# Performance work log

Measured on AMD Instinct MI355X. Metric: run time of the kernel, lower is better.

Reference implementation:

```python
import jax, jax.numpy as jnp
import numpy as np

NUM_HEADS = 8
NUM_LEVELS = 4
NUM_POINTS = 4


def _grid_sample(v, grid):
    """Bilinear grid_sample, padding_mode='zeros', align_corners=False.
    v: (N, C, H, W), grid: (N, Hg, Wg, 2) with grid[...,0]=x, grid[...,1]=y in [-1,1].
    Returns (N, C, Hg, Wg)."""
    N, C, H, W = v.shape
    Hg, Wg = grid.shape[1], grid.shape[2]
    x = ((grid[..., 0] + 1.0) * W - 1.0) * 0.5
    y = ((grid[..., 1] + 1.0) * H - 1.0) * 0.5
    x0 = jnp.floor(x)
    y0 = jnp.floor(y)
    x1 = x0 + 1.0
    y1 = y0 + 1.0
    wx1 = x - x0
    wx0 = 1.0 - wx1
    wy1 = y - y0
    wy0 = 1.0 - wy1
    vf = v.reshape(N, C, H * W)

    def corner(xi, yi, w):
        valid = (xi >= 0) & (xi < W) & (yi >= 0) & (yi < H)
        xi_c = jnp.clip(xi, 0, W - 1).astype(jnp.int32)
        yi_c = jnp.clip(yi, 0, H - 1).astype(jnp.int32)
        idx = (yi_c * W + xi_c).reshape(N, 1, Hg * Wg)
        g = jnp.take_along_axis(vf, idx, axis=2).reshape(N, C, Hg, Wg)
        return g * (w * valid.astype(v.dtype))[:, None]

    return (corner(x0, y0, wx0 * wy0) + corner(x1, y0, wx1 * wy0)
            + corner(x0, y1, wx0 * wy1) + corner(x1, y1, wx1 * wy1))


def setup_inputs() -> dict:
    rng = jax.random.key(0)
    ks = jax.random.split(rng, 6)
    bs, num_q, embed = 1, 40000, 256
    num_kv = NUM_LEVELS * NUM_POINTS  # 16, enforced by the module's asserts
    return {
        "query": jax.random.normal(ks[0], (bs, num_q, embed), jnp.float32),
        "key": jax.random.normal(ks[1], (bs, num_kv, embed), jnp.float32),
        "value": jax.random.normal(ks[2], (bs, num_kv, embed), jnp.float32),
        "reference_points": jax.random.uniform(ks[3], (bs, num_q, NUM_LEVELS, 2), jnp.float32),
        "spatial_shapes": np.array([[1, 2], [2, 2], [2, 3], [1, 2]], dtype=np.int32),  # (h,w), sums to 16
        "W_so": jax.random.normal(ks[4], (embed, NUM_HEADS * NUM_LEVELS * NUM_POINTS * 2), jnp.float32) * 0.02,
        "b_so": jax.random.normal(ks[5], (NUM_HEADS * NUM_LEVELS * NUM_POINTS * 2,), jnp.float32) * 0.02,
    }


def reference(query, key, value, reference_points, spatial_shapes, W_so, b_so):
    b, nq, embed = query.shape
    h, l, p = NUM_HEADS, NUM_LEVELS, NUM_POINTS
    d = embed // h
    ss = np.asarray(spatial_shapes)  # static (l, 2) (h, w)

    # sampling offsets: (b, nq, h, p, l, 2)  -- note (p, l) order per the original view
    off = (query @ W_so + b_so).reshape(b, nq, h, p, l, 2)

    # NOTE: to_Q/to_K/to_V outputs are overwritten in the original (dead code);
    # attention uses the raw query/key reshaped per-head.
    q = query.reshape(b, nq, h, d)
    k = key.reshape(b, -1, h, d)
    v = value.reshape(b, -1, h, d)
    attn = jax.nn.softmax(jnp.einsum('bqhd,bkhd->bqhk', q, k), axis=-1)
    attn = attn.reshape(b, nq, h, l, p)

    # normalize offsets by (w, h) per level, add reference points, then
    # reinterpret (p, l) axes as (l, p) via a plain reshape (faithful to .view)
    norm = jnp.asarray(np.stack([ss[:, 1], ss[:, 0]], axis=-1), dtype=query.dtype)  # (l, 2)
    loc = reference_points[:, :, None, None, :, :] + off / norm  # (b, nq, h, p, l, 2)
    loc = loc.reshape(b, nq, h, l, p, 2)
    grids = 2.0 * loc - 1.0

    sampled = []
    start = 0
    for lev in range(l):
        H_, W_ = int(ss[lev, 0]), int(ss[lev, 1])
        v_l = v[:, start:start + H_ * W_].transpose(0, 2, 3, 1).reshape(b * h, d, H_, W_)
        start += H_ * W_
        g_l = grids[:, :, :, lev].transpose(0, 2, 1, 3, 4).reshape(b * h, nq, p, 2)
        sampled.append(_grid_sample(v_l, g_l))  # (b*h, d, nq, p)
    sampled = jnp.stack(sampled, axis=-2).reshape(b * h, d, nq, l * p)

    aw = attn.transpose(0, 2, 1, 3, 4).reshape(b * h, 1, nq, l * p)
    out = (sampled * aw).sum(-1).reshape(b, h * d, nq)
    return out.transpose(0, 2, 1)
```

## Files before the change

kernel.cpp:

```cpp
#include <hip/hip_runtime.h>
#include <hip/hip_bf16.h>
#include <stdint.h>


typedef __attribute__((ext_vector_type(8))) short short8;
typedef __attribute__((ext_vector_type(4))) float float4_;

#define SB_OFF 5120
#define LDSTR 40
#define SMEM_BYTES 32768

static __device__ __forceinline__ uint16_t f2bf(float f) {
    union { float f; uint32_t u; } a; a.f = f;
    uint32_t r = a.u + 0x7fffu + ((a.u >> 16) & 1u);
    return (uint16_t)(r >> 16);
}
static __device__ __forceinline__ float bf2f(uint16_t b) {
    union { uint32_t u; float f; } a; a.u = ((uint32_t)b) << 16;
    return a.f;
}

template <int H_, int W_, int ST_>
static __device__ __forceinline__ void scatter(float* ws, float a, float x, float y) {
    float x0f = floorf(x), y0f = floorf(y);
    float fx = x - x0f, fy = y - y0f;
    int ix0 = (int)x0f, iy0 = (int)y0f;
    float xc[W_], yc[H_];
#pragma unroll
    for (int cx = 0; cx < W_; ++cx)
        xc[cx] = (ix0 == cx) ? (1.f - fx) : ((ix0 + 1 == cx) ? fx : 0.f);
#pragma unroll
    for (int cy = 0; cy < H_; ++cy)
        yc[cy] = ((iy0 == cy) ? (1.f - fy) : ((iy0 + 1 == cy) ? fy : 0.f)) * a;
#pragma unroll
    for (int cy = 0; cy < H_; ++cy)
#pragma unroll
        for (int cx = 0; cx < W_; ++cx)
            ws[ST_ + cy * W_ + cx] += xc[cx] * yc[cy];
}

__global__ __launch_bounds__(256) void k_transpose(const float* __restrict__ W,
                                                   uint16_t* __restrict__ WTb) {
    int n = blockIdx.x, k = threadIdx.x;
    WTb[n * 256 + k] = f2bf(W[k * 256 + n]);
}

__global__ __launch_bounds__(512, 4) void k_fused(const float* __restrict__ q,
                                                  const float* __restrict__ key,
                                                  const float* __restrict__ value,
                                                  const float* __restrict__ refp,
                                                  const uint16_t* __restrict__ WTb,
                                                  const float* __restrict__ bso,
                                                  float* __restrict__ out) {
    __shared__ __align__(16) char smem[SMEM_BYTES];
    short* sA = (short*)smem;
    short* sB = (short*)(smem + SB_OFF);

    int t = threadIdx.x;
    int w = t >> 6, l = t & 63;
    int qbase = blockIdx.x * 64;
    int qa = qbase + l;
    int g = l >> 4, lrow = l & 15, lk = g * 8;

    int wm = w >> 2, wn = w & 3;
    int ar = t >> 3, ak = t & 7;
    int bn = t >> 1, bh = (t & 1) * 16;
    float4_ acc[2][4];
#pragma unroll
    for (int i = 0; i < 2; ++i)
#pragma unroll
        for (int j = 0; j < 4; ++j) acc[i][j] = (float4_)0.f;

    for (int ks = 0; ks < 8; ++ks) {
        __syncthreads();
        {
            float4_ v = *(const float4_*)(q + (size_t)(qbase + ar) * 256 + ks * 32 + ak * 4);
            uint32_t p0 = (uint32_t)f2bf(v.x) | ((uint32_t)f2bf(v.y) << 16);
            uint32_t p1 = (uint32_t)f2bf(v.z) | ((uint32_t)f2bf(v.w) << 16);
            uint32_t* dst = (uint32_t*)&sA[ar * LDSTR + ak * 4];
            dst[0] = p0; dst[1] = p1;
        }
        {
            const short8* src = (const short8*)(WTb + bn * 256 + ks * 32 + bh);
            *(short8*)&sB[bn * LDSTR + bh]     = src[0];
            *(short8*)&sB[bn * LDSTR + bh + 8] = src[1];
        }
        __syncthreads();
        short8 af[2], bf[4];
#pragma unroll
        for (int mi = 0; mi < 2; ++mi)
            af[mi] = *(const short8*)&sA[(wm * 32 + mi * 16 + lrow) * LDSTR + lk];
#pragma unroll
        for (int ni = 0; ni < 4; ++ni)
            bf[ni] = *(const short8*)&sB[(wn * 64 + ni * 16 + lrow) * LDSTR + lk];
#pragma unroll
        for (int mi = 0; mi < 2; ++mi)
#pragma unroll
            for (int ni = 0; ni < 4; ++ni)
                acc[mi][ni] = __builtin_amdgcn_mfma_f32_16x16x32_bf16(
                    af[mi], bf[ni], acc[mi][ni], 0, 0, 0);
    }
    __syncthreads();

#pragma unroll
    for (int mi = 0; mi < 2; ++mi)
#pragma unroll
        for (int ni = 0; ni < 4; ++ni) {
            int col = wn * 64 + ni * 16 + lrow;
            float b = bso[col];
            int qrow = wm * 32 + mi * 16 + g * 4;
#pragma unroll
            for (int r = 0; r < 4; ++r) {
                int row = qrow + r;
                *(uint16_t*)(smem + row * 512 + ((col * 2) ^ ((row & 7) << 4))) =
                    f2bf(acc[mi][ni][r] + b);
            }
        }

    float sc[16];
    {
        const float4_* qp = (const float4_*)(q + (size_t)qa * 256 + w * 32);
        float4_ qv[8];
#pragma unroll
        for (int j = 0; j < 8; ++j) qv[j] = qp[j];
#pragma unroll
        for (int kk = 0; kk < 16; ++kk) {
            const float4_* kp = (const float4_*)(key + kk * 256 + w * 32);
            float a = 0.f;
#pragma unroll
            for (int j = 0; j < 8; ++j) {
                float4_ kv = kp[j];
                a += qv[j].x * kv.x + qv[j].y * kv.y + qv[j].z * kv.z + qv[j].w * kv.w;
            }
            sc[kk] = a;
        }
        float m = sc[0];
#pragma unroll
        for (int kk = 1; kk < 16; ++kk) m = fmaxf(m, sc[kk]);
        float s = 0.f;
#pragma unroll
        for (int kk = 0; kk < 16; ++kk) { sc[kk] = __expf(sc[kk] - m); s += sc[kk]; }
        float inv = 1.f / s;
#pragma unroll
        for (int kk = 0; kk < 16; ++kk) sc[kk] *= inv;
    }
    __syncthreads();

    union OvU { short8 v; short s[8]; } ov[4];
#pragma unroll
    for (int i = 0; i < 4; ++i)
        ov[i].v = *(const short8*)(smem + l * 512 + ((w * 64 + i * 16) ^ ((l & 7) << 4)));

    union VbU { short8 v; uint16_t u[8]; } vb[2];
#pragma unroll
    for (int nt = 0; nt < 2; ++nt) {
        if (g < 2) {
            int col = w * 32 + nt * 16 + lrow;
#pragma unroll
            for (int j = 0; j < 8; ++j)
                vb[nt].u[j] = f2bf(value[(g * 8 + j) * 256 + col]);
        } else {
#pragma unroll
            for (int j = 0; j < 8; ++j) vb[nt].u[j] = 0;
        }
    }

    float4_ r01 = *(const float4_*)(refp + (size_t)qa * 8);
    float4_ r23 = *(const float4_*)(refp + (size_t)qa * 8 + 4);
    float rx[4] = {r01.x, r01.z, r23.x, r23.z};
    float ry[4] = {r01.y, r01.w, r23.y, r23.w};

    float ws[14];
#pragma unroll
    for (int j = 0; j < 14; ++j) ws[j] = 0.f;

#define SAMPLE_LP(LP, PP, GH, GW, ST, NW, NH)                                 \
    {                                                                         \
        float ox = bf2f((uint16_t)ov[(2 * (LP)) >> 3].s[(2 * (LP)) & 7]);     \
        float oy = bf2f((uint16_t)ov[(2 * (LP) + 1) >> 3].s[(2 * (LP) + 1) & 7]); \
        float x = (rx[PP] + ox * (NW)) * (float)(GW)-0.5f;                    \
        float y = (ry[PP] + oy * (NH)) * (float)(GH)-0.5f;                    \
        scatter<GH, GW, ST>(ws, sc[LP], x, y);                                \
    }
    SAMPLE_LP(0, 0, 1, 2, 0, 0.5f, 1.0f)
    SAMPLE_LP(1, 1, 1, 2, 0, 0.5f, 0.5f)
    SAMPLE_LP(2, 2, 1, 2, 0, (1.f / 3.f), 0.5f)
    SAMPLE_LP(3, 3, 1, 2, 0, 0.5f, 1.0f)
    SAMPLE_LP(4, 0, 2, 2, 2, 0.5f, 1.0f)
    SAMPLE_LP(5, 1, 2, 2, 2, 0.5f, 0.5f)
    SAMPLE_LP(6, 2, 2, 2, 2, (1.f / 3.f), 0.5f)
    SAMPLE_LP(7, 3, 2, 2, 2, 0.5f, 1.0f)
    SAMPLE_LP(8, 0, 2, 3, 6, 0.5f, 1.0f)
    SAMPLE_LP(9, 1, 2, 3, 6, 0.5f, 0.5f)
    SAMPLE_LP(10, 2, 2, 3, 6, (1.f / 3.f), 0.5f)
    SAMPLE_LP(11, 3, 2, 3, 6, 0.5f, 1.0f)
    SAMPLE_LP(12, 0, 1, 2, 12, 0.5f, 1.0f)
    SAMPLE_LP(13, 1, 1, 2, 12, 0.5f, 0.5f)
    SAMPLE_LP(14, 2, 1, 2, 12, (1.f / 3.f), 0.5f)
    SAMPLE_LP(15, 3, 1, 2, 12, 0.5f, 1.0f)
#undef SAMPLE_LP

    __syncthreads();

    {
        union PkU { uint32_t u[8]; short8 v2[2]; } pk;
#pragma unroll
        for (int j = 0; j < 7; ++j)
            pk.u[j] = (uint32_t)f2bf(ws[2 * j]) | ((uint32_t)f2bf(ws[2 * j + 1]) << 16);
        pk.u[7] = 0;
        *(short8*)(smem + t * 48)      = pk.v2[0];
        *(short8*)(smem + t * 48 + 16) = pk.v2[1];
    }
    __syncthreads();

    {
        union ZU { uint32_t u[4]; short8 v; } az;
        az.u[0] = 0; az.u[1] = 0; az.u[2] = 0; az.u[3] = 0;
        float4_ acc2[4][2];
#pragma unroll
        for (int i = 0; i < 4; ++i)
#pragma unroll
            for (int j = 0; j < 2; ++j) acc2[i][j] = (float4_)0.f;
#pragma unroll
        for (int mt = 0; mt < 4; ++mt) {
            short8 af = (g < 2)
                ? *(const short8*)(smem + (w * 64 + mt * 16 + lrow) * 48 + g * 16)
                : az.v;
#pragma unroll
            for (int nt = 0; nt < 2; ++nt)
                acc2[mt][nt] = __builtin_amdgcn_mfma_f32_16x16x32_bf16(
                    af, vb[nt].v, acc2[mt][nt], 0, 0, 0);
        }
#pragma unroll
        for (int mt = 0; mt < 4; ++mt)
#pragma unroll
            for (int nt = 0; nt < 2; ++nt)
#pragma unroll
                for (int r = 0; r < 4; ++r)
                    out[(size_t)(qbase + mt * 16 + g * 4 + r) * 256
                        + w * 32 + nt * 16 + lrow] = acc2[mt][nt][r];
    }
}

extern "C" void kernel_launch(void* const* d_in, const int* in_sizes, int n_in,
                              void* d_out, int out_size, void* d_ws, size_t ws_size,
                              hipStream_t stream) {
    (void)in_sizes; (void)n_in; (void)out_size; (void)ws_size;
    const float* query = (const float*)d_in[0];
    const float* key   = (const float*)d_in[1];
    const float* value = (const float*)d_in[2];
    const float* refp  = (const float*)d_in[3];
    const float* Wso   = (const float*)d_in[5];
    const float* bso   = (const float*)d_in[6];
    uint16_t* WTb = (uint16_t*)d_ws;

    hipLaunchKernelGGL(k_transpose, dim3(256), dim3(256), 0, stream, Wso, WTb);
    hipLaunchKernelGGL(k_fused, dim3(625), dim3(512), 0, stream,
                       query, key, value, refp, WTb, bso, (float*)d_out);
}
```

Before: 70.51 us.

## Halve query tile to 32 per block and register-prefetch next GEMM k-slice

Each block now handles 32 queries with 256 threads instead of 64 queries with 512, doubling the grid to 1250 blocks and cutting LDS use so more blocks fit per CU. The q and W tiles for the next k-step are loaded into registers while the current step computes, hiding global latency behind the MFMA work. Work is remapped so each thread covers a (query, head) pair and each wave does two heads in the value MFMA stage. The cost is that W tiles are reloaded by twice as many blocks, and value is converted twice per wave.

```diff
diff --git a/kernel.cpp b/kernel.cpp
--- a/kernel.cpp
+++ b/kernel.cpp
@@ -6,9 +6,9 @@
 typedef __attribute__((ext_vector_type(8))) short short8;
 typedef __attribute__((ext_vector_type(4))) float float4_;
 
-#define SB_OFF 5120
 #define LDSTR 40
-#define SMEM_BYTES 32768
+#define SB_OFF 2560
+#define SMEM_BYTES 23040
 
 static __device__ __forceinline__ uint16_t f2bf(float f) {
     union { float f; uint32_t u; } a; a.f = f;
@@ -45,7 +45,7 @@
     WTb[n * 256 + k] = f2bf(W[k * 256 + n]);
 }
 
-__global__ __launch_bounds__(512, 4) void k_fused(const float* __restrict__ q,
+__global__ __launch_bounds__(256, 6) void k_fused(const float* __restrict__ q,
                                                   const float* __restrict__ key,
                                                   const float* __restrict__ value,
                                                   const float* __restrict__ refp,
@@ -58,41 +58,49 @@
 
     int t = threadIdx.x;
     int w = t >> 6, l = t & 63;
-    int qbase = blockIdx.x * 64;
-    int qa = qbase + l;
     int g = l >> 4, lrow = l & 15, lk = g * 8;
-
-    int wm = w >> 2, wn = w & 3;
+    int qbase = blockIdx.x * 32;
+    int h2 = t >> 5, ql = t & 31;
+    int qa = qbase + ql;
+
     int ar = t >> 3, ak = t & 7;
-    int bn = t >> 1, bh = (t & 1) * 16;
     float4_ acc[2][4];
 #pragma unroll
     for (int i = 0; i < 2; ++i)
 #pragma unroll
         for (int j = 0; j < 4; ++j) acc[i][j] = (float4_)0.f;
+
+    float4_ pa = *(const float4_*)(q + (size_t)(qbase + ar) * 256 + ak * 4);
+    short8 pb[4];
+#pragma unroll
+    for (int j = 0; j < 4; ++j)
+        pb[j] = *(const short8*)(WTb + t * 256 + j * 8);
 
     for (int ks = 0; ks < 8; ++ks) {
         __syncthreads();
         {
-            float4_ v = *(const float4_*)(q + (size_t)(qbase + ar) * 256 + ks * 32 + ak * 4);
-            uint32_t p0 = (uint32_t)f2bf(v.x) | ((uint32_t)f2bf(v.y) << 16);
-            uint32_t p1 = (uint32_t)f2bf(v.z) | ((uint32_t)f2bf(v.w) << 16);
+            uint32_t p0 = (uint32_t)f2bf(pa.x) | ((uint32_t)f2bf(pa.y) << 16);
+            uint32_t p1 = (uint32_t)f2bf(pa.z) | ((uint32_t)f2bf(pa.w) << 16);
             uint32_t* dst = (uint32_t*)&sA[ar * LDSTR + ak * 4];
             dst[0] = p0; dst[1] = p1;
-        }
-        {
-            const short8* src = (const short8*)(WTb + bn * 256 + ks * 32 + bh);
-            *(short8*)&sB[bn * LDSTR + bh]     = src[0];
-            *(short8*)&sB[bn * LDSTR + bh + 8] = src[1];
+#pragma unroll
+            for (int j = 0; j < 4; ++j)
+                *(short8*)&sB[t * LDSTR + j * 8] = pb[j];
+        }
+        if (ks < 7) {
+            pa = *(const float4_*)(q + (size_t)(qbase + ar) * 256 + (ks + 1) * 32 + ak * 4);
+#pragma unroll
+            for (int j = 0; j < 4; ++j)
+                pb[j] = *(const short8*)(WTb + t * 256 + (ks + 1) * 32 + j * 8);
         }
         __syncthreads();
         short8 af[2], bf[4];
 #pragma unroll
         for (int mi = 0; mi < 2; ++mi)
-            af[mi] = *(const short8*)&sA[(wm * 32 + mi * 16 + lrow) * LDSTR + lk];
+            af[mi] = *(const short8*)&sA[(mi * 16 + lrow) * LDSTR + lk];
 #pragma unroll
         for (int ni = 0; ni < 4; ++ni)
-            bf[ni] = *(const short8*)&sB[(wn * 64 + ni * 16 + lrow) * LDSTR + lk];
+            bf[ni] = *(const short8*)&sB[(w * 64 + ni * 16 + lrow) * LDSTR + lk];
 #pragma unroll
         for (int mi = 0; mi < 2; ++mi)
 #pragma unroll
@@ -106,9 +114,9 @@
     for (int mi = 0; mi < 2; ++mi)
 #pragma unroll
         for (int ni = 0; ni < 4; ++ni) {
-            int col = wn * 64 + ni * 16 + lrow;
+            int col = w * 64 + ni * 16 + lrow;
             float b = bso[col];
-            int qrow = wm * 32 + mi * 16 + g * 4;
+            int qrow = mi * 16 + g * 4;
 #pragma unroll
             for (int r = 0; r < 4; ++r) {
                 int row = qrow + r;
@@ -118,22 +126,27 @@
         }
 
     float sc[16];
-    {
-        const float4_* qp = (const float4_*)(q + (size_t)qa * 256 + w * 32);
-        float4_ qv[8];
-#pragma unroll
-        for (int j = 0; j < 8; ++j) qv[j] = qp[j];
+#pragma unroll
+    for (int kk = 0; kk < 16; ++kk) sc[kk] = 0.f;
+#pragma unroll
+    for (int half = 0; half < 2; ++half) {
+        const float4_* qp = (const float4_*)(q + (size_t)qa * 256 + h2 * 32 + half * 16);
+        float4_ qv[4];
+#pragma unroll
+        for (int j = 0; j < 4; ++j) qv[j] = qp[j];
 #pragma unroll
         for (int kk = 0; kk < 16; ++kk) {
-            const float4_* kp = (const float4_*)(key + kk * 256 + w * 32);
+            const float4_* kp = (const float4_*)(key + kk * 256 + h2 * 32 + half * 16);
             float a = 0.f;
 #pragma unroll
-            for (int j = 0; j < 8; ++j) {
+            for (int j = 0; j < 4; ++j) {
                 float4_ kv = kp[j];
                 a += qv[j].x * kv.x + qv[j].y * kv.y + qv[j].z * kv.z + qv[j].w * kv.w;
             }
-            sc[kk] = a;
-        }
+            sc[kk] += a;
+        }
+    }
+    {
         float m = sc[0];
 #pragma unroll
         for (int kk = 1; kk < 16; ++kk) m = fmaxf(m, sc[kk]);
@@ -149,21 +162,7 @@
     union OvU { short8 v; short s[8]; } ov[4];
 #pragma unroll
     for (int i = 0; i < 4; ++i)
-        ov[i].v = *(const short8*)(smem + l * 512 + ((w * 64 + i * 16) ^ ((l & 7) << 4)));
-
-    union VbU { short8 v; uint16_t u[8]; } vb[2];
-#pragma unroll
-    for (int nt = 0; nt < 2; ++nt) {
-        if (g < 2) {
-            int col = w * 32 + nt * 16 + lrow;
-#pragma unroll
-            for (int j = 0; j < 8; ++j)
-                vb[nt].u[j] = f2bf(value[(g * 8 + j) * 256 + col]);
-        } else {
-#pragma unroll
-            for (int j = 0; j < 8; ++j) vb[nt].u[j] = 0;
-        }
-    }
+        ov[i].v = *(const short8*)(smem + ql * 512 + ((h2 * 64 + i * 16) ^ ((ql & 7) << 4)));
 
     float4_ r01 = *(const float4_*)(refp + (size_t)qa * 8);
     float4_ r23 = *(const float4_*)(refp + (size_t)qa * 8 + 4);
@@ -174,13 +173,13 @@
 #pragma unroll
     for (int j = 0; j < 14; ++j) ws[j] = 0.f;
 
-#define SAMPLE_LP(LP, PP, GH, GW, ST, NW, NH)                                 \
-    {                                                                         \
-        float ox = bf2f((uint16_t)ov[(2 * (LP)) >> 3].s[(2 * (LP)) & 7]);     \
+#define SAMPLE_LP(LP, PP, GH, GW, ST, NW, NH)                                     \
+    {                                                                             \
+        float ox = bf2f((uint16_t)ov[(2 * (LP)) >> 3].s[(2 * (LP)) & 7]);         \
         float oy = bf2f((uint16_t)ov[(2 * (LP) + 1) >> 3].s[(2 * (LP) + 1) & 7]); \
-        float x = (rx[PP] + ox * (NW)) * (float)(GW)-0.5f;                    \
-        float y = (ry[PP] + oy * (NH)) * (float)(GH)-0.5f;                    \
-        scatter<GH, GW, ST>(ws, sc[LP], x, y);                                \
+        float x = (rx[PP] + ox * (NW)) * (float)(GW)-0.5f;                        \
+        float y = (ry[PP] + oy * (NH)) * (float)(GH)-0.5f;                        \
+        scatter<GH, GW, ST>(ws, sc[LP], x, y);                                    \
     }
     SAMPLE_LP(0, 0, 1, 2, 0, 0.5f, 1.0f)
     SAMPLE_LP(1, 1, 1, 2, 0, 0.5f, 0.5f)
@@ -216,29 +215,45 @@
     {
         union ZU { uint32_t u[4]; short8 v; } az;
         az.u[0] = 0; az.u[1] = 0; az.u[2] = 0; az.u[3] = 0;
-        float4_ acc2[4][2];
-#pragma unroll
-        for (int i = 0; i < 4; ++i)
-#pragma unroll
-            for (int j = 0; j < 2; ++j) acc2[i][j] = (float4_)0.f;
-#pragma unroll
-        for (int mt = 0; mt < 4; ++mt) {
-            short8 af = (g < 2)
-                ? *(const short8*)(smem + (w * 64 + mt * 16 + lrow) * 48 + g * 16)
-                : az.v;
-#pragma unroll
-            for (int nt = 0; nt < 2; ++nt)
-                acc2[mt][nt] = __builtin_amdgcn_mfma_f32_16x16x32_bf16(
-                    af, vb[nt].v, acc2[mt][nt], 0, 0, 0);
-        }
-#pragma unroll
-        for (int mt = 0; mt < 4; ++mt)
-#pragma unroll
-            for (int nt = 0; nt < 2; ++nt)
-#pragma unroll
-                for (int r = 0; r < 4; ++r)
-                    out[(size_t)(qbase + mt * 16 + g * 4 + r) * 256
-                        + w * 32 + nt * 16 + lrow] = acc2[mt][nt][r];
+#pragma unroll
+        for (int hh = 0; hh < 2; ++hh) {
+            int h = 2 * w + hh;
+            union VbU { short8 v; uint16_t u[8]; } vb[2];
+#pragma unroll
+            for (int nt = 0; nt < 2; ++nt) {
+                if (g < 2) {
+                    int col = h * 32 + nt * 16 + lrow;
+#pragma unroll
+                    for (int j = 0; j < 8; ++j)
+                        vb[nt].u[j] = f2bf(value[(g * 8 + j) * 256 + col]);
+                } else {
+                    vb[nt].v = az.v;
+                }
+            }
+            float4_ acc2[2][2];
+#pragma unroll
+            for (int i = 0; i < 2; ++i)
+#pragma unroll
+                for (int j = 0; j < 2; ++j) acc2[i][j] = (float4_)0.f;
+#pragma unroll
+            for (int mt = 0; mt < 2; ++mt) {
+                short8 af = (g < 2)
+                    ? *(const short8*)(smem + (h * 32 + mt * 16 + lrow) * 48 + g * 16)
+                    : az.v;
+#pragma unroll
+                for (int nt = 0; nt < 2; ++nt)
+                    acc2[mt][nt] = __builtin_amdgcn_mfma_f32_16x16x32_bf16(
+                        af, vb[nt].v, acc2[mt][nt], 0, 0, 0);
+            }
+#pragma unroll
+            for (int mt = 0; mt < 2; ++mt)
+#pragma unroll
+                for (int nt = 0; nt < 2; ++nt)
+#pragma unroll
+                    for (int r = 0; r < 4; ++r)
+                        out[(size_t)(qbase + mt * 16 + g * 4 + r) * 256
+                            + h * 32 + nt * 16 + lrow] = acc2[mt][nt][r];
+        }
     }
 }
 
@@ -255,6 +270,6 @@
     uint16_t* WTb = (uint16_t*)d_ws;
 
     hipLaunchKernelGGL(k_transpose, dim3(256), dim3(256), 0, stream, Wso, WTb);
-    hipLaunchKernelGGL(k_fused, dim3(625), dim3(512), 0, stream,
+    hipLaunchKernelGGL(k_fused, dim3(1250), dim3(256), 0, stream,
                        query, key, value, refp, WTb, bso, (float*)d_out);
 }
```

After: 167.4 us. +137.4%, slower.

## Restructure into single-wave blocks with pre-swizzled MFMA fragment tables for W and value

Applied to the files above, without the earlier changes.

A prep kernel now converts W_so and value into bf16 tables already in MFMA B-fragment order. The fused kernel runs as one 64-thread wave per 16 queries instead of 512 threads per 64 queries. It reads B fragments straight from global memory with no LDS staging or barriers, and each lane handles two heads for softmax and sampling. This removes block-wide syncs and LDS tiling of the projection, and raises the block count. In exchange, W fragments are re-read from global/L2 by every block and the work per wave grows.

```diff
diff --git a/kernel.cpp b/kernel.cpp
--- a/kernel.cpp
+++ b/kernel.cpp
@@ -6,9 +6,9 @@
 typedef __attribute__((ext_vector_type(8))) short short8;
 typedef __attribute__((ext_vector_type(4))) float float4_;
 
-#define SB_OFF 5120
-#define LDSTR 40
-#define SMEM_BYTES 32768
+#define SOFF_B 0
+#define WSF_B 8192
+#define SMEM_BYTES 14336
 
 static __device__ __forceinline__ uint16_t f2bf(float f) {
     union { float f; uint32_t u; } a; a.f = f;
@@ -39,129 +39,73 @@
             ws[ST_ + cy * W_ + cx] += xc[cx] * yc[cy];
 }
 
-__global__ __launch_bounds__(256) void k_transpose(const float* __restrict__ W,
-                                                   uint16_t* __restrict__ WTb) {
-    int n = blockIdx.x, k = threadIdx.x;
-    WTb[n * 256 + k] = f2bf(W[k * 256 + n]);
-}
-
-__global__ __launch_bounds__(512, 4) void k_fused(const float* __restrict__ q,
-                                                  const float* __restrict__ key,
-                                                  const float* __restrict__ value,
-                                                  const float* __restrict__ refp,
-                                                  const uint16_t* __restrict__ WTb,
-                                                  const float* __restrict__ bso,
-                                                  float* __restrict__ out) {
+__global__ __launch_bounds__(256) void k_prep(const float* __restrict__ W,
+                                              const float* __restrict__ value,
+                                              uint16_t* __restrict__ tab) {
+    int tid = threadIdx.x, b = blockIdx.x;
+    if (b < 32) {
+        int f = b * 256 + tid;
+        int l = f & 63, nt = (f >> 6) & 15, ks = (f >> 10) & 7;
+        int col = nt * 16 + (l & 15);
+        int kb = ks * 32 + (l >> 4) * 8;
+        uint16_t* dst = tab + (size_t)f * 8;
+#pragma unroll
+        for (int j = 0; j < 8; ++j) dst[j] = f2bf(W[(size_t)(kb + j) * 256 + col]);
+    } else {
+        int f = (b - 32) * 256 + tid;
+        int l = f & 63, nt2 = f >> 6;
+        int col = nt2 * 16 + (l & 15);
+        int g = l >> 4;
+        uint16_t* dst = tab + 65536 + (size_t)f * 8;
+#pragma unroll
+        for (int j = 0; j < 8; ++j)
+            dst[j] = (g < 2) ? f2bf(value[(size_t)(g * 8 + j) * 256 + col]) : (uint16_t)0;
+    }
+}
+
+__global__ __launch_bounds__(64) void k_fused(const float* __restrict__ q,
+                                              const float* __restrict__ key,
+                                              const float* __restrict__ refp,
+                                              const uint16_t* __restrict__ Wfrag,
+                                              const uint16_t* __restrict__ vfrag,
+                                              const float* __restrict__ bso,
+                                              float* __restrict__ out) {
     __shared__ __align__(16) char smem[SMEM_BYTES];
-    short* sA = (short*)smem;
-    short* sB = (short*)(smem + SB_OFF);
-
-    int t = threadIdx.x;
-    int w = t >> 6, l = t & 63;
-    int qbase = blockIdx.x * 64;
-    int qa = qbase + l;
-    int g = l >> 4, lrow = l & 15, lk = g * 8;
-
-    int wm = w >> 2, wn = w & 3;
-    int ar = t >> 3, ak = t & 7;
-    int bn = t >> 1, bh = (t & 1) * 16;
-    float4_ acc[2][4];
-#pragma unroll
-    for (int i = 0; i < 2; ++i)
-#pragma unroll
-        for (int j = 0; j < 4; ++j) acc[i][j] = (float4_)0.f;
-
-    for (int ks = 0; ks < 8; ++ks) {
-        __syncthreads();
-        {
-            float4_ v = *(const float4_*)(q + (size_t)(qbase + ar) * 256 + ks * 32 + ak * 4);
-            uint32_t p0 = (uint32_t)f2bf(v.x) | ((uint32_t)f2bf(v.y) << 16);
-            uint32_t p1 = (uint32_t)f2bf(v.z) | ((uint32_t)f2bf(v.w) << 16);
-            uint32_t* dst = (uint32_t*)&sA[ar * LDSTR + ak * 4];
-            dst[0] = p0; dst[1] = p1;
-        }
-        {
-            const short8* src = (const short8*)(WTb + bn * 256 + ks * 32 + bh);
-            *(short8*)&sB[bn * LDSTR + bh]     = src[0];
-            *(short8*)&sB[bn * LDSTR + bh + 8] = src[1];
-        }
-        __syncthreads();
-        short8 af[2], bf[4];
-#pragma unroll
-        for (int mi = 0; mi < 2; ++mi)
-            af[mi] = *(const short8*)&sA[(wm * 32 + mi * 16 + lrow) * LDSTR + lk];
-#pragma unroll
-        for (int ni = 0; ni < 4; ++ni)
-            bf[ni] = *(const short8*)&sB[(wn * 64 + ni * 16 + lrow) * LDSTR + lk];
-#pragma unroll
-        for (int mi = 0; mi < 2; ++mi)
-#pragma unroll
-            for (int ni = 0; ni < 4; ++ni)
-                acc[mi][ni] = __builtin_amdgcn_mfma_f32_16x16x32_bf16(
-                    af[mi], bf[ni], acc[mi][ni], 0, 0, 0);
-    }
-    __syncthreads();
-
-#pragma unroll
-    for (int mi = 0; mi < 2; ++mi)
-#pragma unroll
-        for (int ni = 0; ni < 4; ++ni) {
-            int col = wn * 64 + ni * 16 + lrow;
-            float b = bso[col];
-            int qrow = wm * 32 + mi * 16 + g * 4;
-#pragma unroll
-            for (int r = 0; r < 4; ++r) {
-                int row = qrow + r;
-                *(uint16_t*)(smem + row * 512 + ((col * 2) ^ ((row & 7) << 4))) =
-                    f2bf(acc[mi][ni][r] + b);
+    int l = threadIdx.x;
+    int g = l >> 4, lr = l & 15;
+    int qb = blockIdx.x * 16;
+    int qa = qb + lr;
+
+    for (int np = 0; np < 2; ++np) {
+        float4_ acc[8];
+#pragma unroll
+        for (int i = 0; i < 8; ++i) acc[i] = (float4_)0.f;
+#pragma unroll
+        for (int ks = 0; ks < 8; ++ks) {
+            const float4_* ap = (const float4_*)(q + (size_t)(qb + lr) * 256 + ks * 32 + g * 8);
+            float4_ a0 = ap[0], a1 = ap[1];
+            union { uint32_t u[4]; short8 v; } af;
+            af.u[0] = (uint32_t)f2bf(a0.x) | ((uint32_t)f2bf(a0.y) << 16);
+            af.u[1] = (uint32_t)f2bf(a0.z) | ((uint32_t)f2bf(a0.w) << 16);
+            af.u[2] = (uint32_t)f2bf(a1.x) | ((uint32_t)f2bf(a1.y) << 16);
+            af.u[3] = (uint32_t)f2bf(a1.z) | ((uint32_t)f2bf(a1.w) << 16);
+#pragma unroll
+            for (int nt = 0; nt < 8; ++nt) {
+                short8 bf = *(const short8*)(Wfrag
+                    + ((size_t)(ks * 16 + np * 8 + nt) * 64 + l) * 8);
+                acc[nt] = __builtin_amdgcn_mfma_f32_16x16x32_bf16(af.v, bf, acc[nt], 0, 0, 0);
             }
         }
-
-    float sc[16];
-    {
-        const float4_* qp = (const float4_*)(q + (size_t)qa * 256 + w * 32);
-        float4_ qv[8];
-#pragma unroll
-        for (int j = 0; j < 8; ++j) qv[j] = qp[j];
-#pragma unroll
-        for (int kk = 0; kk < 16; ++kk) {
-            const float4_* kp = (const float4_*)(key + kk * 256 + w * 32);
-            float a = 0.f;
-#pragma unroll
-            for (int j = 0; j < 8; ++j) {
-                float4_ kv = kp[j];
-                a += qv[j].x * kv.x + qv[j].y * kv.y + qv[j].z * kv.z + qv[j].w * kv.w;
+#pragma unroll
+        for (int nt = 0; nt < 8; ++nt) {
+            int col = (np * 8 + nt) * 16 + lr;
+            float b = bso[col];
+#pragma unroll
+            for (int r = 0; r < 4; ++r) {
+                int row = g * 4 + r;
+                *(uint16_t*)(smem + SOFF_B + row * 512 + ((col * 2) ^ ((row & 7) << 4))) =
+                    f2bf(acc[nt][r] + b);
             }
-            sc[kk] = a;
-        }
-        float m = sc[0];
-#pragma unroll
-        for (int kk = 1; kk < 16; ++kk) m = fmaxf(m, sc[kk]);
-        float s = 0.f;
-#pragma unroll
-        for (int kk = 0; kk < 16; ++kk) { sc[kk] = __expf(sc[kk] - m); s += sc[kk]; }
-        float inv = 1.f / s;
-#pragma unroll
-        for (int kk = 0; kk < 16; ++kk) sc[kk] *= inv;
-    }
-    __syncthreads();
-
-    union OvU { short8 v; short s[8]; } ov[4];
-#pragma unroll
-    for (int i = 0; i < 4; ++i)
-        ov[i].v = *(const short8*)(smem + l * 512 + ((w * 64 + i * 16) ^ ((l & 7) << 4)));
-
-    union VbU { short8 v; uint16_t u[8]; } vb[2];
-#pragma unroll
-    for (int nt = 0; nt < 2; ++nt) {
-        if (g < 2) {
-            int col = w * 32 + nt * 16 + lrow;
-#pragma unroll
-            for (int j = 0; j < 8; ++j)
-                vb[nt].u[j] = f2bf(value[(g * 8 + j) * 256 + col]);
-        } else {
-#pragma unroll
-            for (int j = 0; j < 8; ++j) vb[nt].u[j] = 0;
         }
     }
 
@@ -170,75 +114,122 @@
     float rx[4] = {r01.x, r01.z, r23.x, r23.z};
     float ry[4] = {r01.y, r01.w, r23.y, r23.w};
 
-    float ws[14];
-#pragma unroll
-    for (int j = 0; j < 14; ++j) ws[j] = 0.f;
-
-#define SAMPLE_LP(LP, PP, GH, GW, ST, NW, NH)                                 \
+    float wsA[14], wsB[14];
+
+#define SAMPLE_PT(WS, J, PP, GH, GW, ST, NW, NH)                              \
     {                                                                         \
-        float ox = bf2f((uint16_t)ov[(2 * (LP)) >> 3].s[(2 * (LP)) & 7]);     \
-        float oy = bf2f((uint16_t)ov[(2 * (LP) + 1) >> 3].s[(2 * (LP) + 1) & 7]); \
+        float ox = bf2f((uint16_t)ovl.s[2 * (J)]);                            \
+        float oy = bf2f((uint16_t)ovl.s[2 * (J) + 1]);                        \
         float x = (rx[PP] + ox * (NW)) * (float)(GW)-0.5f;                    \
         float y = (ry[PP] + oy * (NH)) * (float)(GH)-0.5f;                    \
-        scatter<GH, GW, ST>(ws, sc[LP], x, y);                                \
-    }
-    SAMPLE_LP(0, 0, 1, 2, 0, 0.5f, 1.0f)
-    SAMPLE_LP(1, 1, 1, 2, 0, 0.5f, 0.5f)
-    SAMPLE_LP(2, 2, 1, 2, 0, (1.f / 3.f), 0.5f)
-    SAMPLE_LP(3, 3, 1, 2, 0, 0.5f, 1.0f)
-    SAMPLE_LP(4, 0, 2, 2, 2, 0.5f, 1.0f)
-    SAMPLE_LP(5, 1, 2, 2, 2, 0.5f, 0.5f)
-    SAMPLE_LP(6, 2, 2, 2, 2, (1.f / 3.f), 0.5f)
-    SAMPLE_LP(7, 3, 2, 2, 2, 0.5f, 1.0f)
-    SAMPLE_LP(8, 0, 2, 3, 6, 0.5f, 1.0f)
-    SAMPLE_LP(9, 1, 2, 3, 6, 0.5f, 0.5f)
-    SAMPLE_LP(10, 2, 2, 3, 6, (1.f / 3.f), 0.5f)
-    SAMPLE_LP(11, 3, 2, 3, 6, 0.5f, 1.0f)
-    SAMPLE_LP(12, 0, 1, 2, 12, 0.5f, 1.0f)
-    SAMPLE_LP(13, 1, 1, 2, 12, 0.5f, 0.5f)
-    SAMPLE_LP(14, 2, 1, 2, 12, (1.f / 3.f), 0.5f)
-    SAMPLE_LP(15, 3, 1, 2, 12, 0.5f, 1.0f)
-#undef SAMPLE_LP
-
-    __syncthreads();
+        scatter<GH, GW, ST>(WS, sc[4 * LEV + (J)], x, y);                     \
+    }
+#define DO_PASS(WS, HH)                                                           \
+    {                                                                             \
+        const int h = (HH);                                                       \
+        float sc[16];                                                             \
+        {                                                                         \
+            const float4_* qp = (const float4_*)(q + (size_t)qa * 256 + h * 32);  \
+            float4_ qv[8];                                                        \
+            _Pragma("unroll") for (int j = 0; j < 8; ++j) qv[j] = qp[j];          \
+            _Pragma("unroll") for (int kk = 0; kk < 16; ++kk) {                   \
+                const float4_* kp = (const float4_*)(key + kk * 256 + h * 32);    \
+                float a = 0.f;                                                    \
+                _Pragma("unroll") for (int j = 0; j < 8; ++j) {                   \
+                    float4_ kv = kp[j];                                           \
+                    a += qv[j].x * kv.x + qv[j].y * kv.y + qv[j].z * kv.z         \
+                       + qv[j].w * kv.w;                                          \
+                }                                                                 \
+                sc[kk] = a;                                                       \
+            }                                                                     \
+            float m = sc[0];                                                      \
+            _Pragma("unroll") for (int kk = 1; kk < 16; ++kk) m = fmaxf(m, sc[kk]); \
+            float s = 0.f;                                                        \
+            _Pragma("unroll") for (int kk = 0; kk < 16; ++kk) {                   \
+                sc[kk] = __expf(sc[kk] - m); s += sc[kk];                         \
+            }                                                                     \
+            float inv = 1.f / s;                                                  \
+            _Pragma("unroll") for (int kk = 0; kk < 16; ++kk) sc[kk] *= inv;      \
+        }                                                                         \
+        _Pragma("unroll") for (int j = 0; j < 14; ++j) WS[j] = 0.f;               \
+        union OvU { short8 v; short s[8]; } ovl;                                  \
+        {                                                                         \
+            enum { LEV = 0 };                                                     \
+            ovl.v = *(const short8*)(smem + SOFF_B + lr * 512                     \
+                        + ((h * 64 + LEV * 16) ^ ((lr & 7) << 4)));               \
+            SAMPLE_PT(WS, 0, 0, 1, 2, 0, 0.5f, 1.0f)                              \
+            SAMPLE_PT(WS, 1, 1, 1, 2, 0, 0.5f, 0.5f)                              \
+            SAMPLE_PT(WS, 2, 2, 1, 2, 0, (1.f / 3.f), 0.5f)                       \
+            SAMPLE_PT(WS, 3, 3, 1, 2, 0, 0.5f, 1.0f)                              \
+        }                                                                         \
+        {                                                                         \
+            enum { LEV = 1 };                                                     \
+            ovl.v = *(const short8*)(smem + SOFF_B + lr * 512                     \
+                        + ((h * 64 + LEV * 16) ^ ((lr & 7) << 4)));               \
+            SAMPLE_PT(WS, 0, 0, 2, 2, 2, 0.5f, 1.0f)                              \
+            SAMPLE_PT(WS, 1, 1, 2, 2, 2, 0.5f, 0.5f)                              \
+            SAMPLE_PT(WS, 2, 2, 2, 2, 2, (1.f / 3.f), 0.5f)                       \
+            SAMPLE_PT(WS, 3, 3, 2, 2, 2, 0.5f, 1.0f)                              \
+        }                                                                         \
+        {                                                                         \
+            enum { LEV = 2 };                                                     \
+            ovl.v = *(const short8*)(smem + SOFF_B + lr * 512                     \
+                        + ((h * 64 + LEV * 16) ^ ((lr & 7) << 4)));               \
+            SAMPLE_PT(WS, 0, 0, 2, 3, 6, 0.5f, 1.0f)                              \
+            SAMPLE_PT(WS, 1, 1, 2, 3, 6, 0.5f, 0.5f)                              \
+            SAMPLE_PT(WS, 2, 2, 2, 3, 6, (1.f / 3.f), 0.5f)                       \
+            SAMPLE_PT(WS, 3, 3, 2, 3, 6, 0.5f, 1.0f)                              \
+        }                                                                         \
+        {                                                                         \
+            enum { LEV = 3 };                                                     \
+            ovl.v = *(const short8*)(smem + SOFF_B + lr * 512                     \
+                        + ((h * 64 + LEV * 16) ^ ((lr & 7) << 4)));               \
+            SAMPLE_PT(WS, 0, 0, 1, 2, 12, 0.5f, 1.0f)                             \
+            SAMPLE_PT(WS, 1, 1, 1, 2, 12, 0.5f, 0.5f)                             \
+            SAMPLE_PT(WS, 2, 2, 1, 2, 12, (1.f / 3.f), 0.5f)                      \
+            SAMPLE_PT(WS, 3, 3, 1, 2, 12, 0.5f, 1.0f)                             \
+        }                                                                         \
+    }
+
+    DO_PASS(wsA, g)
+    DO_PASS(wsB, g + 4)
+#undef DO_PASS
+#undef SAMPLE_PT
 
     {
         union PkU { uint32_t u[8]; short8 v2[2]; } pk;
 #pragma unroll
         for (int j = 0; j < 7; ++j)
-            pk.u[j] = (uint32_t)f2bf(ws[2 * j]) | ((uint32_t)f2bf(ws[2 * j + 1]) << 16);
+            pk.u[j] = (uint32_t)f2bf(wsA[2 * j]) | ((uint32_t)f2bf(wsA[2 * j + 1]) << 16);
         pk.u[7] = 0;
-        *(short8*)(smem + t * 48)      = pk.v2[0];
-        *(short8*)(smem + t * 48 + 16) = pk.v2[1];
-    }
-    __syncthreads();
+        *(short8*)(smem + WSF_B + g * 768 + lr * 48)      = pk.v2[0];
+        *(short8*)(smem + WSF_B + g * 768 + lr * 48 + 16) = pk.v2[1];
+#pragma unroll
+        for (int j = 0; j < 7; ++j)
+            pk.u[j] = (uint32_t)f2bf(wsB[2 * j]) | ((uint32_t)f2bf(wsB[2 * j + 1]) << 16);
+        pk.u[7] = 0;
+        *(short8*)(smem + WSF_B + (g + 4) * 768 + lr * 48)      = pk.v2[0];
+        *(short8*)(smem + WSF_B + (g + 4) * 768 + lr * 48 + 16) = pk.v2[1];
+    }
 
     {
         union ZU { uint32_t u[4]; short8 v; } az;
         az.u[0] = 0; az.u[1] = 0; az.u[2] = 0; az.u[3] = 0;
-        float4_ acc2[4][2];
-#pragma unroll
-        for (int i = 0; i < 4; ++i)
-#pragma unroll
-            for (int j = 0; j < 2; ++j) acc2[i][j] = (float4_)0.f;
-#pragma unroll
-        for (int mt = 0; mt < 4; ++mt) {
-            short8 af = (g < 2)
-                ? *(const short8*)(smem + (w * 64 + mt * 16 + lrow) * 48 + g * 16)
+        float4_ z4 = (float4_)0.f;
+#pragma unroll
+        for (int hp = 0; hp < 8; ++hp) {
+            short8 af2 = (g < 2)
+                ? *(const short8*)(smem + WSF_B + hp * 768 + lr * 48 + g * 16)
                 : az.v;
 #pragma unroll
-            for (int nt = 0; nt < 2; ++nt)
-                acc2[mt][nt] = __builtin_amdgcn_mfma_f32_16x16x32_bf16(
-                    af, vb[nt].v, acc2[mt][nt], 0, 0, 0);
+            for (int nt2 = 0; nt2 < 2; ++nt2) {
+                short8 vb = *(const short8*)(vfrag + ((size_t)(hp * 2 + nt2) * 64 + l) * 8);
+                float4_ o = __builtin_amdgcn_mfma_f32_16x16x32_bf16(af2, vb, z4, 0, 0, 0);
+#pragma unroll
+                for (int r = 0; r < 4; ++r)
+                    out[(size_t)(qb + g * 4 + r) * 256 + hp * 32 + nt2 * 16 + lr] = o[r];
+            }
         }
-#pragma unroll
-        for (int mt = 0; mt < 4; ++mt)
-#pragma unroll
-            for (int nt = 0; nt < 2; ++nt)
-#pragma unroll
-                for (int r = 0; r < 4; ++r)
-                    out[(size_t)(qbase + mt * 16 + g * 4 + r) * 256
-                        + w * 32 + nt * 16 + lrow] = acc2[mt][nt][r];
     }
 }
 
@@ -252,9 +243,9 @@
     const float* refp  = (const float*)d_in[3];
     const float* Wso   = (const float*)d_in[5];
     const float* bso   = (const float*)d_in[6];
-    uint16_t* WTb = (uint16_t*)d_ws;
-
-    hipLaunchKernelGGL(k_transpose, dim3(256), dim3(256), 0, stream, Wso, WTb);
-    hipLaunchKernelGGL(k_fused, dim3(625), dim3(512), 0, stream,
-                       query, key, value, refp, WTb, bso, (float*)d_out);
-}
+    uint16_t* tab = (uint16_t*)d_ws;
+
+    hipLaunchKernelGGL(k_prep, dim3(36), dim3(256), 0, stream, Wso, value, tab);
+    hipLaunchKernelGGL(k_fused, dim3(2500), dim3(64), 0, stream,
+                       query, key, refp, tab, tab + 65536, bso, (float*)d_out);
+}
```

Result: slower. 130.1 us (+84.5%).
